# Optimization experiments

Hardware: AMD Instinct MI355X
Metric: run time of the kernel (lower is better)

## Reference

```python
import jax, jax.numpy as jnp
import numpy as np

SCALE = 1.0  # Scaler(scale=1.0) is a fixed multiplicative scale


def setup_inputs() -> dict:
    key = jax.random.key(0)
    ks = jax.random.split(key, 7)
    d = 2048          # in_features == out_features (per-head proj dim)
    out_total = 3 * d # fused QKV weight rows
    r = 8             # LoRA rank
    B, S = 4, 2048
    return {
        "x": jax.random.normal(ks[0], (B, S, d), dtype=jnp.float32),
        "W": jax.random.normal(ks[1], (out_total, d), dtype=jnp.float32) * 0.02,
        "b": jax.random.normal(ks[2], (out_total,), dtype=jnp.float32) * 0.02,
        "A1": jax.random.normal(ks[3], (r, d), dtype=jnp.float32) * 0.02,
        "B1": jax.random.normal(ks[4], (d, r), dtype=jnp.float32) * 0.02,
        "A2": jax.random.normal(ks[5], (r, d), dtype=jnp.float32) * 0.02,
        "B2": jax.random.normal(ks[6], (d, r), dtype=jnp.float32) * 0.02,
    }


def reference(x, W, b, A1, B1, A2, B2):
    # Low-rank deltas for K and V rows: each [out_features, in_features]
    dK = SCALE * (B1 @ A1)            # [d, d]
    dV = SCALE * (B2 @ A2)            # [d, d]
    delta = jnp.concatenate([dK, dV], axis=0)          # [2d, d]
    # zero-pad on top to match full fused weight (Q rows untouched)
    pad_rows = W.shape[0] - delta.shape[0]
    delta_full = jnp.concatenate(
        [jnp.zeros((pad_rows, W.shape[1]), dtype=W.dtype), delta], axis=0
    )                                                    # [3d, d]
    weight = W + delta_full
    # F.linear: x @ weight.T + b
    return jnp.einsum("bsd,od->bso", x, weight) + b
```

## Files before the change

kernel.cpp:

```cpp
#include <hip/hip_runtime.h>
#include <hip/hip_bf16.h>
#include <stdint.h>
#include <stddef.h>

typedef __attribute__((ext_vector_type(8)))  __bf16 bf16x8;
typedef __attribute__((ext_vector_type(16))) float  f32x16;
typedef __attribute__((ext_vector_type(8)))  unsigned short ushort8;

typedef const void __attribute__((address_space(1)))* as1_cvp;
typedef void       __attribute__((address_space(3)))* as3_vp;

__device__ __forceinline__ void gload_lds16(const void* g, void* l) {
    __builtin_amdgcn_global_load_lds((as1_cvp)g, (as3_vp)l, 16, 0, 0);
}

__device__ __forceinline__ unsigned short f2bf(float f) {
    union { float f; unsigned u; } v; v.f = f;
    unsigned r = v.u + 0x7fffu + ((v.u >> 16) & 1u);
    return (unsigned short)(r >> 16);
}

__global__ __launch_bounds__(256) void prep_kernel(
    const float* __restrict__ x,
    const float* __restrict__ W,
    const float* __restrict__ A1, const float* __restrict__ B1,
    const float* __restrict__ A2, const float* __restrict__ B2,
    unsigned short* __restrict__ Xb, unsigned short* __restrict__ Wb,
    int d, int nW, int n8)
{
    int blk = blockIdx.x;
    if (blk < nW) {
        int o  = blk;
        int k0 = threadIdx.x * 8;
        const float4* wrow = (const float4*)(W + (size_t)o * d + k0);
        float4 w0 = wrow[0], w1 = wrow[1];
        float acc[8] = {w0.x, w0.y, w0.z, w0.w, w1.x, w1.y, w1.z, w1.w};
        if (o >= d) {
            const float* A  = (o < 2 * d) ? A1 : A2;
            const float* Bm = (o < 2 * d) ? B1 : B2;
            int r0 = o - ((o < 2 * d) ? d : 2 * d);
#pragma unroll
            for (int r = 0; r < 8; ++r) {
                float bb = Bm[(size_t)r0 * 8 + r];
                const float4* arow = (const float4*)(A + (size_t)r * d + k0);
                float4 a0 = arow[0], a1 = arow[1];
                acc[0] += bb * a0.x; acc[1] += bb * a0.y;
                acc[2] += bb * a0.z; acc[3] += bb * a0.w;
                acc[4] += bb * a1.x; acc[5] += bb * a1.y;
                acc[6] += bb * a1.z; acc[7] += bb * a1.w;
            }
        }
        ushort8 ov;
#pragma unroll
        for (int c = 0; c < 8; ++c) ov[c] = f2bf(acc[c]);
        ((ushort8*)(Wb + (size_t)o * d))[threadIdx.x] = ov;
    } else {
        int i = (blk - nW) * 256 + threadIdx.x;
        if (i >= n8) return;
        const float4* s = (const float4*)x + (size_t)i * 2;
        float4 a = s[0], c = s[1];
        ushort8 o;
        o[0] = f2bf(a.x); o[1] = f2bf(a.y); o[2] = f2bf(a.z); o[3] = f2bf(a.w);
        o[4] = f2bf(c.x); o[5] = f2bf(c.y); o[6] = f2bf(c.z); o[7] = f2bf(c.w);
        ((ushort8*)Xb)[i] = o;
    }
}

constexpr int BM = 256, BN = 256, BK = 64;
constexpr int KK = 2048, NN = 6144;
constexpr int TT = KK / BK;

__global__ __launch_bounds__(512, 2) void gemm256_kernel(
    const unsigned short* __restrict__ Xb,
    const unsigned short* __restrict__ Wb,
    const float* __restrict__ bias,
    float* __restrict__ out,
    int M)
{
    __shared__ __align__(16) unsigned short As[2][BM * BK];
    __shared__ __align__(16) unsigned short Bs[2][BN * BK];

    const int tid  = threadIdx.x;
    const int wave = tid >> 6;
    const int lane = tid & 63;
    const int half = lane >> 5;
    const int ln32 = lane & 31;
    const int wrow = wave >> 2;
    const int wcol = wave & 3;

    int nwg = (int)gridDim.x;
    int bid = (int)blockIdx.x;
    int swz = bid;
    if ((nwg & 7) == 0) swz = (bid & 7) * (nwg >> 3) + (bid >> 3);
    const int ntn = NN / BN;
    const int bm = (swz / ntn) * BM;
    const int bn = (swz % ntn) * BN;

    const int rtid = tid >> 3;
    const int ctid = (tid & 7) ^ (rtid & 7);
    const size_t gA0 = (size_t)(bm + rtid) * KK + ctid * 8;
    const size_t gB0 = (size_t)(bn + rtid) * KK + ctid * 8;
    const int ldsW = wave * 512;

#define STAGE_A(t, j, buf) gload_lds16(Xb + gA0 + (size_t)(j) * 64 * KK + (size_t)(t) * BK, \
                                       &As[(buf)][(j) * 4096 + ldsW])
#define STAGE_B(t, j, buf) gload_lds16(Wb + gB0 + (size_t)(j) * 64 * KK + (size_t)(t) * BK, \
                                       &Bs[(buf)][(j) * 4096 + ldsW])

    const int r7 = ln32 & 7;
    int dofs[4];
#pragma unroll
    for (int s = 0; s < 4; ++s) dofs[s] = ((s * 2 + half) ^ r7) * 8;
    int baseA[2][2];
#pragma unroll
    for (int qm = 0; qm < 2; ++qm)
#pragma unroll
        for (int f = 0; f < 2; ++f)
            baseA[qm][f] = (wrow * 128 + qm * 64 + f * 32 + ln32) * BK;
    int baseB[2];
#pragma unroll
    for (int qn = 0; qn < 2; ++qn) baseB[qn] = (wcol * 64 + qn * 32 + ln32) * BK;

    f32x16 acc[4][2];
#pragma unroll
    for (int i = 0; i < 4; ++i)
#pragma unroll
        for (int j = 0; j < 2; ++j)
#pragma unroll
            for (int r = 0; r < 16; ++r) acc[i][j][r] = 0.f;

    bf16x8 a0f[2][4], a1f[2][4], b0[4], b1[4];

#define LOAD_AQ(SRC, qm, DST) do { _Pragma("unroll") for (int s = 0; s < 4; ++s) {  \
        DST[0][s] = *(const bf16x8*)&(SRC)[baseA[qm][0] + dofs[s]];                 \
        DST[1][s] = *(const bf16x8*)&(SRC)[baseA[qm][1] + dofs[s]]; } } while (0)
#define LOAD_BQ(SRC, qn, DST) do { _Pragma("unroll") for (int s = 0; s < 4; ++s) {  \
        DST[s] = *(const bf16x8*)&(SRC)[baseB[qn] + dofs[s]]; } } while (0)
#define MFMA_CL(AF, i0, i1, jj, BB) do {                                            \
        __builtin_amdgcn_s_setprio(1);                                             \
        _Pragma("unroll") for (int s = 0; s < 4; ++s) {                            \
            acc[i0][jj] = __builtin_amdgcn_mfma_f32_32x32x16_bf16(AF[0][s], BB[s], acc[i0][jj], 0, 0, 0); \
            acc[i1][jj] = __builtin_amdgcn_mfma_f32_32x32x16_bf16(AF[1][s], BB[s], acc[i1][jj], 0, 0, 0); \
        }                                                                          \
        __builtin_amdgcn_s_setprio(0); } while (0)
#define BAR() asm volatile("s_barrier" ::: "memory")

#define GROUP(v, QQ, SN1, SN2, VMW, RN) do {                                       \
        const unsigned short* Aq  = &As[(QQ)][0];                                  \
        const unsigned short* Bq  = &Bs[(QQ)][0];                                  \
        const unsigned short* Aq2 = &As[(QQ) ^ 1][0];                              \
        const unsigned short* Bq2 = &Bs[(QQ) ^ 1][0];                              \
                  \
        LOAD_BQ(Bq, 1, b1);                                                        \
        if (SN1) { STAGE_B((v) + 1, 2, (QQ) ^ 1); STAGE_B((v) + 1, 3, (QQ) ^ 1); } \
        BAR();                                                                     \
        MFMA_CL(a0f, 0, 1, 0, b0);                                                 \
        BAR();                                                                     \
                                       \
        LOAD_AQ(Aq, 1, a1f);                                                       \
        if (SN1) { STAGE_A((v) + 1, 1, (QQ) ^ 1); STAGE_A((v) + 1, 3, (QQ) ^ 1); } \
        BAR();                                                                     \
        MFMA_CL(a0f, 0, 1, 1, b1);                                                 \
        BAR();                                                                     \
                                                       \
        if (SN2) { STAGE_A((v) + 2, 0, (QQ)); STAGE_A((v) + 2, 2, (QQ)); }         \
        BAR();                                                                     \
        MFMA_CL(a1f, 2, 3, 0, b0);                                                 \
        BAR();                                                                     \
               \
        if (SN2) { STAGE_B((v) + 2, 0, (QQ)); STAGE_B((v) + 2, 1, (QQ)); }         \
        if ((VMW) == 4)      asm volatile("s_waitcnt vmcnt(4)" ::: "memory");      \
        else if ((VMW) == 0) asm volatile("s_waitcnt vmcnt(0)" ::: "memory");      \
        BAR();                                                                     \
        if (RN) { LOAD_AQ(Aq2, 0, a0f); LOAD_BQ(Bq2, 0, b0); }                     \
        MFMA_CL(a1f, 2, 3, 1, b1);                                                 \
        BAR();                                                                     \
    } while (0)

#pragma unroll
    for (int j = 0; j < 4; ++j) STAGE_A(0, j, 0);
#pragma unroll
    for (int j = 0; j < 4; ++j) STAGE_B(0, j, 0);
    STAGE_A(1, 0, 1); STAGE_A(1, 2, 1);
    STAGE_B(1, 0, 1); STAGE_B(1, 1, 1);
    asm volatile("s_waitcnt vmcnt(4)" ::: "memory");
    BAR();
    LOAD_AQ((&As[0][0]), 0, a0f);
    LOAD_BQ((&Bs[0][0]), 0, b0);

    for (int vv = 0; vv < TT - 2; vv += 2) {
        GROUP(vv,     0, 1, 1, 4, 1);
        GROUP(vv + 1, 1, 1, 1, 4, 1);
    }
    GROUP(TT - 2, 0, 1, 0, 0, 1);
    GROUP(TT - 1, 1, 0, 0, -1, 0);

#undef GROUP
#undef BAR
#undef MFMA_CL
#undef LOAD_BQ
#undef LOAD_AQ
#undef STAGE_B
#undef STAGE_A

#pragma unroll
    for (int j = 0; j < 2; ++j) {
        int col = bn + wcol * 64 + j * 32 + ln32;
        float bv = bias[col];
#pragma unroll
        for (int i = 0; i < 4; ++i) {
            int rbase = bm + wrow * 128 + i * 32 + 4 * half;
#pragma unroll
            for (int reg = 0; reg < 16; ++reg) {
                int row = rbase + (reg & 3) + 8 * (reg >> 2);
                out[(size_t)row * NN + col] = acc[i][j][reg] + bv;
            }
        }
    }
}

extern "C" void kernel_launch(void* const* d_in, const int* in_sizes, int n_in,
                              void* d_out, int out_size, void* d_ws, size_t ws_size,
                              hipStream_t stream) {
    const float* x  = (const float*)d_in[0];
    const float* W  = (const float*)d_in[1];
    const float* b  = (const float*)d_in[2];
    const float* A1 = (const float*)d_in[3];
    const float* B1 = (const float*)d_in[4];
    const float* A2 = (const float*)d_in[5];
    const float* B2 = (const float*)d_in[6];
    float* out = (float*)d_out;

    const int d = 2048;
    const int K = d;
    const int N = 3 * d;
    const int M = in_sizes[0] / d;

    unsigned short* Xbf = (unsigned short*)d_ws;
    unsigned short* Wbf = Xbf + (size_t)M * K;

    int n8 = (M * K) / 8;
    int castBlocks = (n8 + 255) / 256;
    prep_kernel<<<N + castBlocks, 256, 0, stream>>>(x, W, A1, B1, A2, B2,
                                                    Xbf, Wbf, d, N, n8);

    dim3 grid((M / BM) * (N / BN));
    gemm256_kernel<<<grid, 512, 0, stream>>>(Xbf, Wbf, b, out, M);
}
```

Measured before the change: 531.2 us.

## Switch GEMM inner loop to 16x16x32 MFMA with reordered LDS staging

Replaces the 32x32x16 bf16 MFMA tiling with 16x16x32 MFMA instructions, giving each wave 8x4 accumulator tiles and new fragment load patterns from the swizzled LDS layout. The per-phase staging schedule is reordered so A loads for the next tile are issued first and B loads for tile t+2 later, and the prologue stages all of B for tile 1. The aim is better MFMA issue density and fragment reuse. It drops the cross-group register prefetch of the next tile's fragments, so LDS reads now sit directly before each MFMA phase and may expose latency.

```diff
diff --git a/kernel.cpp b/kernel.cpp
--- a/kernel.cpp
+++ b/kernel.cpp
@@ -4,7 +4,7 @@
 #include <stddef.h>
 
 typedef __attribute__((ext_vector_type(8)))  __bf16 bf16x8;
-typedef __attribute__((ext_vector_type(16))) float  f32x16;
+typedef __attribute__((ext_vector_type(4)))  float  f32x4;
 typedef __attribute__((ext_vector_type(8)))  unsigned short ushort8;
 
 typedef const void __attribute__((address_space(1)))* as1_cvp;
@@ -83,8 +83,8 @@
     const int tid  = threadIdx.x;
     const int wave = tid >> 6;
     const int lane = tid & 63;
-    const int half = lane >> 5;
-    const int ln32 = lane & 31;
+    const int l15  = lane & 15;
+    const int l4   = lane >> 4;
     const int wrow = wave >> 2;
     const int wcol = wave & 3;
 
@@ -107,113 +107,102 @@
 #define STAGE_B(t, j, buf) gload_lds16(Wb + gB0 + (size_t)(j) * 64 * KK + (size_t)(t) * BK, \
                                        &Bs[(buf)][(j) * 4096 + ldsW])
 
-    const int r7 = ln32 & 7;
-    int dofs[4];
-#pragma unroll
-    for (int s = 0; s < 4; ++s) dofs[s] = ((s * 2 + half) ^ r7) * 8;
-    int baseA[2][2];
-#pragma unroll
-    for (int qm = 0; qm < 2; ++qm)
-#pragma unroll
-        for (int f = 0; f < 2; ++f)
-            baseA[qm][f] = (wrow * 128 + qm * 64 + f * 32 + ln32) * BK;
-    int baseB[2];
-#pragma unroll
-    for (int qn = 0; qn < 2; ++qn) baseB[qn] = (wcol * 64 + qn * 32 + ln32) * BK;
-
-    f32x16 acc[4][2];
-#pragma unroll
-    for (int i = 0; i < 4; ++i)
-#pragma unroll
-        for (int j = 0; j < 2; ++j)
-#pragma unroll
-            for (int r = 0; r < 16; ++r) acc[i][j][r] = 0.f;
-
-    bf16x8 a0f[2][4], a1f[2][4], b0[4], b1[4];
-
-#define LOAD_AQ(SRC, qm, DST) do { _Pragma("unroll") for (int s = 0; s < 4; ++s) {  \
-        DST[0][s] = *(const bf16x8*)&(SRC)[baseA[qm][0] + dofs[s]];                 \
-        DST[1][s] = *(const bf16x8*)&(SRC)[baseA[qm][1] + dofs[s]]; } } while (0)
-#define LOAD_BQ(SRC, qn, DST) do { _Pragma("unroll") for (int s = 0; s < 4; ++s) {  \
-        DST[s] = *(const bf16x8*)&(SRC)[baseB[qn] + dofs[s]]; } } while (0)
-#define MFMA_CL(AF, i0, i1, jj, BB) do {                                            \
+    int slotk[2];
+#pragma unroll
+    for (int ks = 0; ks < 2; ++ks) slotk[ks] = ((ks * 4 + l4) ^ (lane & 7)) * 8;
+    const int rowAb = (wrow * 128 + l15) * 64;
+    const int rowBb = (wcol * 64 + l15) * 64;
+
+    f32x4 acc[8][4];
+#pragma unroll
+    for (int i = 0; i < 8; ++i)
+#pragma unroll
+        for (int j = 0; j < 4; ++j)
+#pragma unroll
+            for (int r = 0; r < 4; ++r) acc[i][j][r] = 0.f;
+
+    bf16x8 a[4][2], b0[2][2], b1[2][2];
+
+#define LOAD_A4(SRC, rh) do { _Pragma("unroll") for (int rt = 0; rt < 4; ++rt)      \
+        { _Pragma("unroll") for (int ks = 0; ks < 2; ++ks)                          \
+            a[rt][ks] = *(const bf16x8*)&(SRC)[rowAb + ((rh) * 4 + rt) * 1024 + slotk[ks]]; } } while (0)
+#define LOAD_B2(SRC, ch, DST) do { _Pragma("unroll") for (int c2 = 0; c2 < 2; ++c2) \
+        { _Pragma("unroll") for (int ks = 0; ks < 2; ++ks)                          \
+            DST[c2][ks] = *(const bf16x8*)&(SRC)[rowBb + ((ch) * 2 + c2) * 1024 + slotk[ks]]; } } while (0)
+#define MFMA_PH(rh, ch, BB) do {                                                    \
         __builtin_amdgcn_s_setprio(1);                                             \
-        _Pragma("unroll") for (int s = 0; s < 4; ++s) {                            \
-            acc[i0][jj] = __builtin_amdgcn_mfma_f32_32x32x16_bf16(AF[0][s], BB[s], acc[i0][jj], 0, 0, 0); \
-            acc[i1][jj] = __builtin_amdgcn_mfma_f32_32x32x16_bf16(AF[1][s], BB[s], acc[i1][jj], 0, 0, 0); \
-        }                                                                          \
+        _Pragma("unroll") for (int ks = 0; ks < 2; ++ks)                           \
+        _Pragma("unroll") for (int c2 = 0; c2 < 2; ++c2)                           \
+        _Pragma("unroll") for (int rt = 0; rt < 4; ++rt)                           \
+            acc[(rh) * 4 + rt][(ch) * 2 + c2] = __builtin_amdgcn_mfma_f32_16x16x32_bf16( \
+                a[rt][ks], BB[c2][ks], acc[(rh) * 4 + rt][(ch) * 2 + c2], 0, 0, 0);     \
         __builtin_amdgcn_s_setprio(0); } while (0)
 #define BAR() asm volatile("s_barrier" ::: "memory")
 
-#define GROUP(v, QQ, SN1, SN2, VMW, RN) do {                                       \
-        const unsigned short* Aq  = &As[(QQ)][0];                                  \
-        const unsigned short* Bq  = &Bs[(QQ)][0];                                  \
-        const unsigned short* Aq2 = &As[(QQ) ^ 1][0];                              \
-        const unsigned short* Bq2 = &Bs[(QQ) ^ 1][0];                              \
-                  \
-        LOAD_BQ(Bq, 1, b1);                                                        \
-        if (SN1) { STAGE_B((v) + 1, 2, (QQ) ^ 1); STAGE_B((v) + 1, 3, (QQ) ^ 1); } \
-        BAR();                                                                     \
-        MFMA_CL(a0f, 0, 1, 0, b0);                                                 \
-        BAR();                                                                     \
-                                       \
-        LOAD_AQ(Aq, 1, a1f);                                                       \
-        if (SN1) { STAGE_A((v) + 1, 1, (QQ) ^ 1); STAGE_A((v) + 1, 3, (QQ) ^ 1); } \
-        BAR();                                                                     \
-        MFMA_CL(a0f, 0, 1, 1, b1);                                                 \
-        BAR();                                                                     \
-                                                       \
-        if (SN2) { STAGE_A((v) + 2, 0, (QQ)); STAGE_A((v) + 2, 2, (QQ)); }         \
-        BAR();                                                                     \
-        MFMA_CL(a1f, 2, 3, 0, b0);                                                 \
-        BAR();                                                                     \
-               \
-        if (SN2) { STAGE_B((v) + 2, 0, (QQ)); STAGE_B((v) + 2, 1, (QQ)); }         \
+#define GROUP16(v, QQ, S1, S2, VMW) do {                                           \
+        const unsigned short* Aq = &As[(QQ)][0];                                   \
+        const unsigned short* Bq = &Bs[(QQ)][0];                                   \
+                                                                          \
+        LOAD_A4(Aq, 0); LOAD_B2(Bq, 0, b0);                                        \
+        if (S1) { STAGE_A((v) + 1, 0, (QQ) ^ 1); STAGE_A((v) + 1, 1, (QQ) ^ 1); }  \
+        BAR();                                                                     \
+        MFMA_PH(0, 0, b0);                                                         \
+        BAR();                                                                     \
+                                                                          \
+        LOAD_B2(Bq, 1, b1);                                                        \
+        if (S1) { STAGE_A((v) + 1, 2, (QQ) ^ 1); STAGE_A((v) + 1, 3, (QQ) ^ 1); }  \
+        BAR();                                                                     \
+        MFMA_PH(0, 1, b1);                                                         \
+        BAR();                                                                     \
+                                                                          \
+        LOAD_A4(Aq, 1);                                                            \
+        if (S2) { STAGE_B((v) + 2, 0, (QQ)); STAGE_B((v) + 2, 1, (QQ)); }          \
+        BAR();                                                                     \
+        MFMA_PH(1, 1, b1);                                                         \
+        BAR();                                                                     \
+                                                                          \
+        if (S2) { STAGE_B((v) + 2, 2, (QQ)); STAGE_B((v) + 2, 3, (QQ)); }          \
         if ((VMW) == 4)      asm volatile("s_waitcnt vmcnt(4)" ::: "memory");      \
         else if ((VMW) == 0) asm volatile("s_waitcnt vmcnt(0)" ::: "memory");      \
         BAR();                                                                     \
-        if (RN) { LOAD_AQ(Aq2, 0, a0f); LOAD_BQ(Bq2, 0, b0); }                     \
-        MFMA_CL(a1f, 2, 3, 1, b1);                                                 \
+        MFMA_PH(1, 0, b0);                                                         \
         BAR();                                                                     \
     } while (0)
 
 #pragma unroll
+    for (int j = 0; j < 4; ++j) STAGE_B(0, j, 0);
+#pragma unroll
     for (int j = 0; j < 4; ++j) STAGE_A(0, j, 0);
 #pragma unroll
-    for (int j = 0; j < 4; ++j) STAGE_B(0, j, 0);
-    STAGE_A(1, 0, 1); STAGE_A(1, 2, 1);
-    STAGE_B(1, 0, 1); STAGE_B(1, 1, 1);
+    for (int j = 0; j < 4; ++j) STAGE_B(1, j, 1);
     asm volatile("s_waitcnt vmcnt(4)" ::: "memory");
     BAR();
-    LOAD_AQ((&As[0][0]), 0, a0f);
-    LOAD_BQ((&Bs[0][0]), 0, b0);
 
     for (int vv = 0; vv < TT - 2; vv += 2) {
-        GROUP(vv,     0, 1, 1, 4, 1);
-        GROUP(vv + 1, 1, 1, 1, 4, 1);
+        GROUP16(vv,     0, 1, 1, 4);
+        GROUP16(vv + 1, 1, 1, 1, 4);
     }
-    GROUP(TT - 2, 0, 1, 0, 0, 1);
-    GROUP(TT - 1, 1, 0, 0, -1, 0);
-
-#undef GROUP
+    GROUP16(TT - 2, 0, 1, 0, 0);
+    GROUP16(TT - 1, 1, 0, 0, -1);
+
+#undef GROUP16
 #undef BAR
-#undef MFMA_CL
-#undef LOAD_BQ
-#undef LOAD_AQ
+#undef MFMA_PH
+#undef LOAD_B2
+#undef LOAD_A4
 #undef STAGE_B
 #undef STAGE_A
 
 #pragma unroll
-    for (int j = 0; j < 2; ++j) {
-        int col = bn + wcol * 64 + j * 32 + ln32;
+    for (int ct = 0; ct < 4; ++ct) {
+        int col = bn + wcol * 64 + ct * 16 + l15;
         float bv = bias[col];
 #pragma unroll
-        for (int i = 0; i < 4; ++i) {
-            int rbase = bm + wrow * 128 + i * 32 + 4 * half;
-#pragma unroll
-            for (int reg = 0; reg < 16; ++reg) {
-                int row = rbase + (reg & 3) + 8 * (reg >> 2);
-                out[(size_t)row * NN + col] = acc[i][j][reg] + bv;
+        for (int rt = 0; rt < 8; ++rt) {
+            int rbase = bm + wrow * 128 + rt * 16 + l4 * 4;
+#pragma unroll
+            for (int reg = 0; reg < 4; ++reg) {
+                out[(size_t)(rbase + reg) * NN + col] = acc[rt][ct][reg] + bv;
             }
         }
     }
```

Measured after the change: 470.0 us. -11.5%, faster.
